# Optimization experiments

Hardware: AMD Instinct MI355X
Metric: run time of the kernel (lower is better)

The kernel has to match this reference:

```python
import jax, jax.numpy as jnp
import numpy as np

# ---- static configuration (mirrors scalar_python args) ----
N_SHOTS = 8
NZ = NX = 300
FD_PAD = 2                 # accuracy 4 -> fd_pad = accuracy // 2
NZP = NZ + 2 * FD_PAD      # 304
NXP = NX + 2 * FD_PAD      # 304
NT = 50
N_SRC = 1
N_REC = 300
DT = 0.001
DX = 4.0
INV_DX = 1.0 / DX
INV_DX2 = 1.0 / (DX * DX)
FLAT = NZP * NXP


def _shift(x, axis, s):
    """result[i] = x[i + s] along `axis`, zero-filled outside (matches padded-grid stencil)."""
    n = x.shape[axis]
    pad = [(0, 0)] * x.ndim
    if s > 0:
        xs = jax.lax.slice_in_dim(x, s, n, axis=axis)
        pad[axis] = (0, s)
    else:
        xs = jax.lax.slice_in_dim(x, 0, n + s, axis=axis)
        pad[axis] = (-s, 0)
    return jnp.pad(xs, pad)


def diff1(x, axis):
    """4th-order accurate central first derivative * (1/dx)."""
    return ((_shift(x, axis, 1) - _shift(x, axis, -1)) * (2.0 / 3.0)
            + (_shift(x, axis, -2) - _shift(x, axis, 2)) * (1.0 / 12.0)) * INV_DX


def diff2(x, axis):
    """4th-order accurate central second derivative * (1/dx^2)."""
    return ((-2.5) * x
            + (4.0 / 3.0) * (_shift(x, axis, 1) + _shift(x, axis, -1))
            - (1.0 / 12.0) * (_shift(x, axis, 2) + _shift(x, axis, -2))) * INV_DX2


def _forward_step(v2dt2, wfc, wfp, psi, zeta, a, b, dbdx):
    """One FDTD time step with PML (faithful to deepwave _forward_step, ndim=2)."""
    new_psi, new_zeta = [], []
    w_sum = jnp.zeros_like(wfc)
    for dim in range(2):          # dim 0 = z (axis 1), dim 1 = x (axis 2)
        axis = dim + 1
        dudx = diff1(wfc, axis)
        tmp = ((1.0 + b[dim]) * diff2(wfc, axis)
               + dbdx[dim] * dudx
               + diff1(a[dim] * psi[dim], axis))
        w_sum = w_sum + (1.0 + b[dim]) * tmp + a[dim] * zeta[dim]
        new_psi.append(b[dim] * dudx + a[dim] * psi[dim])
        new_zeta.append(b[dim] * tmp + a[dim] * zeta[dim])
    wfc_new = v2dt2 * w_sum + 2.0 * wfc - wfp
    return wfc_new, new_psi, new_zeta


def setup_inputs() -> dict:
    key = jax.random.key(0)
    ks = jax.random.split(key, 10)
    v = 1500.0 + 1000.0 * jax.random.uniform(ks[0], (NZP, NXP), jnp.float32)
    source_amplitudes = jax.random.normal(ks[1], (NT, N_SHOTS, N_SRC), jnp.float32)
    # PML profiles: (a, b, dbdx) per spatial dim, broadcastable 1D profiles.
    a_z = -0.1 * jax.random.uniform(ks[2], (NZP, 1), jnp.float32)
    b_z = 0.1 * jax.random.uniform(ks[3], (NZP, 1), jnp.float32)
    dbdx_z = 0.01 * jax.random.normal(ks[4], (NZP, 1), jnp.float32)
    a_x = -0.1 * jax.random.uniform(ks[5], (1, NXP), jnp.float32)
    b_x = 0.1 * jax.random.uniform(ks[6], (1, NXP), jnp.float32)
    dbdx_x = 0.01 * jax.random.normal(ks[7], (1, NXP), jnp.float32)
    sources_i = jax.random.randint(ks[8], (N_SHOTS, N_SRC), 0, FLAT, jnp.int32)
    receivers_i = jax.random.randint(ks[9], (N_SHOTS, N_REC), 0, FLAT, jnp.int32)
    return {"v": v, "source_amplitudes": source_amplitudes,
            "a_z": a_z, "b_z": b_z, "dbdx_z": dbdx_z,
            "a_x": a_x, "b_x": b_x, "dbdx_x": dbdx_x,
            "sources_i": sources_i, "receivers_i": receivers_i}


def reference(v, source_amplitudes, a_z, b_z, dbdx_z, a_x, b_x, dbdx_x,
              sources_i, receivers_i):
    v2dt2 = (v * v) * (DT * DT)                 # (NZP, NXP), broadcasts over shots
    a = (a_z, a_x)
    b = (b_z, b_x)
    dbdx = (dbdx_z, dbdx_x)
    shot_idx = jnp.arange(N_SHOTS)[:, None]
    zeros = jnp.zeros((N_SHOTS, NZP, NXP), v.dtype)

    def body(carry, amp_t):
        wfc, wfp, pz, px, zz, zx = carry
        # record receivers from the current wavefield (before the step)
        rec = jnp.take_along_axis(wfc.reshape(N_SHOTS, -1), receivers_i, axis=1)
        wfc_new, (pzn, pxn), (zzn, zxn) = _forward_step(
            v2dt2, wfc, wfp, (pz, px), (zz, zx), a, b, dbdx)
        # inject sources into the new wavefield (scatter-add of flat indices)
        flat = wfc_new.reshape(N_SHOTS, -1).at[shot_idx, sources_i].add(amp_t)
        wfc_new = flat.reshape(N_SHOTS, NZP, NXP)
        return (wfc_new, wfc, pzn, pxn, zzn, zxn), rec

    init = (zeros, zeros, zeros, zeros, zeros, zeros)
    _, receiver_amplitudes = jax.lax.scan(body, init, source_amplitudes)
    return receiver_amplitudes   # (NT, N_SHOTS, N_REC)
```

## Files before the change

### kernel.cpp

```cpp
#include <hip/hip_runtime.h>

#define N_SHOTS 8
#define NZP 304
#define NXP 304
#define NT 50
#define N_REC 300
#define FLAT (NZP * NXP)
#define DT 0.001f
#define INV_DX 0.25f
#define INV_DX2 0.0625f

#define C23 (2.0f / 3.0f)
#define C112 (1.0f / 12.0f)
#define C43 (4.0f / 3.0f)

#define NCH 361

union F4 { float4 v; float f[4]; };
__device__ __forceinline__ F4 ldf4(const float* p) {
    F4 r; r.v = *reinterpret_cast<const float4*>(p); return r;
}
__device__ __forceinline__ F4 zf4() {
    F4 r; r.v = make_float4(0.f, 0.f, 0.f, 0.f); return r;
}

__global__ __launch_bounds__(320) void fdtd_step4(
    const float* __restrict__ v,
    const float* __restrict__ amp,
    const float* __restrict__ az, const float* __restrict__ bz, const float* __restrict__ dbz,
    const float* __restrict__ ax, const float* __restrict__ bx, const float* __restrict__ dbx,
    const int* __restrict__ src_i,
    const int* __restrict__ rec_i,
    const float* __restrict__ wc,
    float* __restrict__ wp,
    const float* __restrict__ pzi, float* __restrict__ pzo,
    const float* __restrict__ pxi, float* __restrict__ pxo,
    float* __restrict__ zz, float* __restrict__ zx,
    float* __restrict__ rec_out,
    int t)
{
    const int bid = blockIdx.x;
    const int shot = bid & 7;
    const int j = bid >> 3;
    const int tid = threadIdx.x;
    const int sbase = shot * FLAT;

    if (tid >= NXP) {
        if (j < 19) {
            int ridx = j * 16 + (tid - NXP);
            if (ridx < N_REC) {
                rec_out[t * (N_SHOTS * N_REC) + shot * N_REC + ridx] =
                    wc[sbase + rec_i[shot * N_REC + ridx]];
            }
        }
        return;
    }

    const int srci = src_i[shot];
    const float amp_t = amp[t * N_SHOTS + shot];
    const int chbase = j * NCH;

    #pragma unroll
    for (int p = 0; p < 2; ++p) {
        const int chl = tid + 304 * p;
        if (p == 1 && tid >= NCH - 304) break;
        const int ch = chbase + chl;
        const int z = ch / 76;
        const int i = ch - z * 76;
        const int x0 = 4 * i;
        const int idx = sbase + 4 * ch;

        const bool lok = (i > 0), rok = (i < 75);
        F4 wCx = ldf4(wc + idx);
        F4 wLx = lok ? ldf4(wc + idx - 4) : zf4();
        F4 wRx = rok ? ldf4(wc + idx + 4) : zf4();
        F4 pCx = ldf4(pxi + idx);
        F4 pLx = lok ? ldf4(pxi + idx - 4) : zf4();
        F4 pRx = rok ? ldf4(pxi + idx + 4) : zf4();
        F4 aCx = ldf4(ax + x0);
        F4 aLx = lok ? ldf4(ax + x0 - 4) : zf4();
        F4 aRx = rok ? ldf4(ax + x0 + 4) : zf4();

        float wx[12], apx[12];
        #pragma unroll
        for (int k = 0; k < 4; ++k) {
            wx[k]     = wLx.f[k];  apx[k]     = aLx.f[k] * pLx.f[k];
            wx[4 + k] = wCx.f[k];  apx[4 + k] = aCx.f[k] * pCx.f[k];
            wx[8 + k] = wRx.f[k];  apx[8 + k] = aRx.f[k] * pRx.f[k];
        }

        const bool m1 = (z >= 1), m2 = (z >= 2), p1 = (z < NZP - 1), p2 = (z < NZP - 2);
        F4 wzm1 = m1 ? ldf4(wc + idx - NXP)     : zf4();
        F4 wzm2 = m2 ? ldf4(wc + idx - 2 * NXP) : zf4();
        F4 wzp1 = p1 ? ldf4(wc + idx + NXP)     : zf4();
        F4 wzp2 = p2 ? ldf4(wc + idx + 2 * NXP) : zf4();
        const float azm1 = m1 ? az[z - 1] : 0.f;
        const float azm2 = m2 ? az[z - 2] : 0.f;
        const float azp1 = p1 ? az[z + 1] : 0.f;
        const float azp2 = p2 ? az[z + 2] : 0.f;
        F4 qzm1 = m1 ? ldf4(pzi + idx - NXP)     : zf4();
        F4 qzm2 = m2 ? ldf4(pzi + idx - 2 * NXP) : zf4();
        F4 qzp1 = p1 ? ldf4(pzi + idx + NXP)     : zf4();
        F4 qzp2 = p2 ? ldf4(pzi + idx + 2 * NXP) : zf4();
        #pragma unroll
        for (int k = 0; k < 4; ++k) {
            qzm1.f[k] *= azm1; qzm2.f[k] *= azm2;
            qzp1.f[k] *= azp1; qzp2.f[k] *= azp2;
        }

        F4 pzC = ldf4(pzi + idx);
        F4 zzC = ldf4(zz + idx);
        F4 zxC = ldf4(zx + idx);
        F4 vC  = ldf4(v + 4 * ch);
        F4 wpC = ldf4(wp + idx);
        F4 bxC = ldf4(bx + x0);
        F4 dxC = ldf4(dbx + x0);
        const float azc = az[z], bzc = bz[z], dbzc = dbz[z];

        F4 o_w, o_pz, o_px, o_zz, o_zx;

        #pragma unroll
        for (int k = 0; k < 4; ++k) {
            const float c = wx[4 + k];
            const float d1x  = ((wx[5 + k] - wx[3 + k]) * C23 + (wx[2 + k] - wx[6 + k]) * C112) * INV_DX;
            const float d2x  = (-2.5f * c + C43 * (wx[5 + k] + wx[3 + k]) - C112 * (wx[6 + k] + wx[2 + k])) * INV_DX2;
            const float dapx = ((apx[5 + k] - apx[3 + k]) * C23 + (apx[2 + k] - apx[6 + k]) * C112) * INV_DX;
            const float d1z  = ((wzp1.f[k] - wzm1.f[k]) * C23 + (wzm2.f[k] - wzp2.f[k]) * C112) * INV_DX;
            const float d2z  = (-2.5f * c + C43 * (wzp1.f[k] + wzm1.f[k]) - C112 * (wzp2.f[k] + wzm2.f[k])) * INV_DX2;
            const float dapz = ((qzp1.f[k] - qzm1.f[k]) * C23 + (qzm2.f[k] - qzp2.f[k]) * C112) * INV_DX;

            const float tmpz = (1.f + bzc) * d2z + dbzc * d1z + dapz;
            float w_sum = (1.f + bzc) * tmpz + azc * zzC.f[k];

            const float bxk = bxC.f[k], axk = aCx.f[k];
            const float tmpx = (1.f + bxk) * d2x + dxC.f[k] * d1x + dapx;
            w_sum += (1.f + bxk) * tmpx + axk * zxC.f[k];

            const float vv = vC.f[k];
            float wn = (vv * vv) * (DT * DT) * w_sum + 2.f * c - wpC.f[k];
            if (4 * ch + k == srci) wn += amp_t;

            o_w.f[k]  = wn;
            o_pz.f[k] = bzc * d1z + azc * pzC.f[k];
            o_px.f[k] = bxk * d1x + apx[4 + k];
            o_zz.f[k] = bzc * tmpz + azc * zzC.f[k];
            o_zx.f[k] = bxk * tmpx + axk * zxC.f[k];
        }

        *reinterpret_cast<float4*>(wp + idx)  = o_w.v;
        *reinterpret_cast<float4*>(pzo + idx) = o_pz.v;
        *reinterpret_cast<float4*>(pxo + idx) = o_px.v;
        *reinterpret_cast<float4*>(zz + idx)  = o_zz.v;
        *reinterpret_cast<float4*>(zx + idx)  = o_zx.v;
    }
}

extern "C" void kernel_launch(void* const* d_in, const int* in_sizes, int n_in,
                              void* d_out, int out_size, void* d_ws, size_t ws_size,
                              hipStream_t stream) {
    const float* v     = (const float*)d_in[0];
    const float* amp   = (const float*)d_in[1];
    const float* az    = (const float*)d_in[2];
    const float* bz    = (const float*)d_in[3];
    const float* dbz   = (const float*)d_in[4];
    const float* ax    = (const float*)d_in[5];
    const float* bx    = (const float*)d_in[6];
    const float* dbx   = (const float*)d_in[7];
    const int* src_i   = (const int*)d_in[8];
    const int* rec_i   = (const int*)d_in[9];
    float* out = (float*)d_out;

    float* ws = (float*)d_ws;
    const size_t A = (size_t)N_SHOTS * FLAT;

    float* wf0 = ws + 0 * A; float* wf1 = ws + 1 * A;
    float* pz0 = ws + 2 * A; float* px0 = ws + 3 * A;
    float* zz  = ws + 4 * A; float* zx  = ws + 5 * A;
    float* pz1 = ws + 6 * A; float* px1 = ws + 7 * A;

    hipMemsetAsync(d_ws, 0, 6 * A * sizeof(float), stream);

    float* wf[2] = { wf0, wf1 };
    float* pz[2] = { pz0, pz1 };
    float* px[2] = { px0, px1 };

    int cur = 0;
    for (int t = 0; t < NT; ++t) {
        fdtd_step4<<<512, 320, 0, stream>>>(
            v, amp, az, bz, dbz, ax, bx, dbx, src_i, rec_i,
            wf[cur], wf[1 - cur],
            pz[cur], pz[1 - cur],
            px[cur], px[1 - cur],
            zz, zx, out, t);
        cur ^= 1;
    }
}
```

Before: 415.3 us.

## Store PML state pre-scaled by a, process two z-rows per thread, cache profiles in LDS

The kernel now keeps the auxiliary fields already multiplied by their PML coefficient a (q = a*psi, a*zeta), so stencil neighbours need no per-point a multiply and az/ax neighbour loads disappear. Each thread handles a 2-row by 4-column tile and reuses a 6-row z window of wavefield and qz loads across both rows, which cuts redundant global reads. The 1D PML profiles are staged in shared memory, and the block size drops to 192. The cost is a __syncthreads per block plus more registers per thread. Numerics shift slightly because the a scaling is folded into stored state.

```diff
diff --git a/kernel.cpp b/kernel.cpp
--- a/kernel.cpp
+++ b/kernel.cpp
@@ -14,7 +14,7 @@
 #define C112 (1.0f / 12.0f)
 #define C43 (4.0f / 3.0f)
 
-#define NCH 361
+#define TPS 11552
 
 union F4 { float4 v; float f[4]; };
 __device__ __forceinline__ F4 ldf4(const float* p) {
@@ -24,7 +24,7 @@
     F4 r; r.v = make_float4(0.f, 0.f, 0.f, 0.f); return r;
 }
 
-__global__ __launch_bounds__(320) void fdtd_step4(
+__global__ __launch_bounds__(192) void fdtd_stepq(
     const float* __restrict__ v,
     const float* __restrict__ amp,
     const float* __restrict__ az, const float* __restrict__ bz, const float* __restrict__ dbz,
@@ -33,125 +33,135 @@
     const int* __restrict__ rec_i,
     const float* __restrict__ wc,
     float* __restrict__ wp,
-    const float* __restrict__ pzi, float* __restrict__ pzo,
-    const float* __restrict__ pxi, float* __restrict__ pxo,
-    float* __restrict__ zz, float* __restrict__ zx,
+    const float* __restrict__ qzi, float* __restrict__ qzo,
+    const float* __restrict__ qxi, float* __restrict__ qxo,
+    float* __restrict__ azz, float* __restrict__ azx,
     float* __restrict__ rec_out,
     int t)
 {
+    __shared__ float laz[NZP], lbz[NZP], ldbz[NZP];
+    __shared__ float4 laxq[76], lbxq[76], ldbxq[76];
+
+    const int tid = threadIdx.x;
     const int bid = blockIdx.x;
     const int shot = bid & 7;
     const int j = bid >> 3;
-    const int tid = threadIdx.x;
     const int sbase = shot * FLAT;
 
-    if (tid >= NXP) {
-        if (j < 19) {
-            int ridx = j * 16 + (tid - NXP);
-            if (ridx < N_REC) {
-                rec_out[t * (N_SHOTS * N_REC) + shot * N_REC + ridx] =
-                    wc[sbase + rec_i[shot * N_REC + ridx]];
-            }
+    for (int p = tid; p < NZP; p += 192) {
+        laz[p] = az[p]; lbz[p] = bz[p]; ldbz[p] = dbz[p];
+    }
+    if (tid < 76) {
+        laxq[tid]  = *reinterpret_cast<const float4*>(ax + 4 * tid);
+        lbxq[tid]  = *reinterpret_cast<const float4*>(bx + 4 * tid);
+        ldbxq[tid] = *reinterpret_cast<const float4*>(dbx + 4 * tid);
+    }
+    __syncthreads();
+
+    if (tid >= 187) {
+        int ridx = j * 5 + (tid - 187);
+        if (ridx < N_REC) {
+            rec_out[t * (N_SHOTS * N_REC) + shot * N_REC + ridx] =
+                wc[sbase + rec_i[shot * N_REC + ridx]];
         }
         return;
     }
 
+    const int start = (j * TPS) >> 6;
+    const int count = (((j + 1) * TPS) >> 6) - start;
+    if (tid >= count) return;
+
+    const int c = start + tid;
+    const int m = c / 76;
+    const int i = c - m * 76;
+    const int z0 = 2 * m;
+    const int x0 = 4 * i;
+    const int idx0 = sbase + z0 * NXP + x0;
+
     const int srci = src_i[shot];
     const float amp_t = amp[t * N_SHOTS + shot];
-    const int chbase = j * NCH;
-
+
+    F4 wCw[6], qzw[6];
     #pragma unroll
-    for (int p = 0; p < 2; ++p) {
-        const int chl = tid + 304 * p;
-        if (p == 1 && tid >= NCH - 304) break;
-        const int ch = chbase + chl;
-        const int z = ch / 76;
-        const int i = ch - z * 76;
-        const int x0 = 4 * i;
-        const int idx = sbase + 4 * ch;
-
-        const bool lok = (i > 0), rok = (i < 75);
-        F4 wCx = ldf4(wc + idx);
-        F4 wLx = lok ? ldf4(wc + idx - 4) : zf4();
-        F4 wRx = rok ? ldf4(wc + idx + 4) : zf4();
-        F4 pCx = ldf4(pxi + idx);
-        F4 pLx = lok ? ldf4(pxi + idx - 4) : zf4();
-        F4 pRx = rok ? ldf4(pxi + idx + 4) : zf4();
-        F4 aCx = ldf4(ax + x0);
-        F4 aLx = lok ? ldf4(ax + x0 - 4) : zf4();
-        F4 aRx = rok ? ldf4(ax + x0 + 4) : zf4();
-
-        float wx[12], apx[12];
+    for (int r = 0; r < 6; ++r) {
+        const int zr = z0 - 2 + r;
+        const bool ok = (zr >= 0) && (zr < NZP);
+        const int a = sbase + zr * NXP + x0;
+        wCw[r] = ok ? ldf4(wc + a)  : zf4();
+        qzw[r] = ok ? ldf4(qzi + a) : zf4();
+    }
+
+    const bool lok = (i > 0), rok = (i < 75);
+    F4 wLr[2], wRr[2], qxL[2], qxC[2], qxR[2];
+    F4 vR[2], wpR[2], azzR[2], azxR[2];
+    #pragma unroll
+    for (int r = 0; r < 2; ++r) {
+        const int a = idx0 + r * NXP;
+        wLr[r] = lok ? ldf4(wc + a - 4)  : zf4();
+        wRr[r] = rok ? ldf4(wc + a + 4)  : zf4();
+        qxC[r] = ldf4(qxi + a);
+        qxL[r] = lok ? ldf4(qxi + a - 4) : zf4();
+        qxR[r] = rok ? ldf4(qxi + a + 4) : zf4();
+        vR[r]   = ldf4(v + (z0 + r) * NXP + x0);
+        wpR[r]  = ldf4(wp + a);
+        azzR[r] = ldf4(azz + a);
+        azxR[r] = ldf4(azx + a);
+    }
+
+    const F4 axv = *(F4*)&laxq[i];
+    const F4 bxv = *(F4*)&lbxq[i];
+    const F4 dxv = *(F4*)&ldbxq[i];
+
+    #pragma unroll
+    for (int r = 0; r < 2; ++r) {
+        const int z = z0 + r;
+        const int idx = idx0 + r * NXP;
+        const float azc = laz[z], bzc = lbz[z], dbzc = ldbz[z];
+        const float azbz = azc * bzc;
+
+        float wx[12], qxw[12];
         #pragma unroll
         for (int k = 0; k < 4; ++k) {
-            wx[k]     = wLx.f[k];  apx[k]     = aLx.f[k] * pLx.f[k];
-            wx[4 + k] = wCx.f[k];  apx[4 + k] = aCx.f[k] * pCx.f[k];
-            wx[8 + k] = wRx.f[k];  apx[8 + k] = aRx.f[k] * pRx.f[k];
+            wx[k]      = wLr[r].f[k];     qxw[k]     = qxL[r].f[k];
+            wx[4 + k]  = wCw[2 + r].f[k]; qxw[4 + k] = qxC[r].f[k];
+            wx[8 + k]  = wRr[r].f[k];     qxw[8 + k] = qxR[r].f[k];
         }
 
-        const bool m1 = (z >= 1), m2 = (z >= 2), p1 = (z < NZP - 1), p2 = (z < NZP - 2);
-        F4 wzm1 = m1 ? ldf4(wc + idx - NXP)     : zf4();
-        F4 wzm2 = m2 ? ldf4(wc + idx - 2 * NXP) : zf4();
-        F4 wzp1 = p1 ? ldf4(wc + idx + NXP)     : zf4();
-        F4 wzp2 = p2 ? ldf4(wc + idx + 2 * NXP) : zf4();
-        const float azm1 = m1 ? az[z - 1] : 0.f;
-        const float azm2 = m2 ? az[z - 2] : 0.f;
-        const float azp1 = p1 ? az[z + 1] : 0.f;
-        const float azp2 = p2 ? az[z + 2] : 0.f;
-        F4 qzm1 = m1 ? ldf4(pzi + idx - NXP)     : zf4();
-        F4 qzm2 = m2 ? ldf4(pzi + idx - 2 * NXP) : zf4();
-        F4 qzp1 = p1 ? ldf4(pzi + idx + NXP)     : zf4();
-        F4 qzp2 = p2 ? ldf4(pzi + idx + 2 * NXP) : zf4();
+        F4 o_w, o_qz, o_qx, o_zz, o_zx;
         #pragma unroll
         for (int k = 0; k < 4; ++k) {
-            qzm1.f[k] *= azm1; qzm2.f[k] *= azm2;
-            qzp1.f[k] *= azp1; qzp2.f[k] *= azp2;
+            const float cc = wx[4 + k];
+            const float d1x  = ((wx[5 + k] - wx[3 + k]) * C23 + (wx[2 + k] - wx[6 + k]) * C112) * INV_DX;
+            const float d2x  = (-2.5f * cc + C43 * (wx[5 + k] + wx[3 + k]) - C112 * (wx[6 + k] + wx[2 + k])) * INV_DX2;
+            const float dapx = ((qxw[5 + k] - qxw[3 + k]) * C23 + (qxw[2 + k] - qxw[6 + k]) * C112) * INV_DX;
+
+            const float d1z  = ((wCw[3 + r].f[k] - wCw[1 + r].f[k]) * C23 + (wCw[r].f[k] - wCw[4 + r].f[k]) * C112) * INV_DX;
+            const float d2z  = (-2.5f * cc + C43 * (wCw[3 + r].f[k] + wCw[1 + r].f[k]) - C112 * (wCw[4 + r].f[k] + wCw[r].f[k])) * INV_DX2;
+            const float dapz = ((qzw[3 + r].f[k] - qzw[1 + r].f[k]) * C23 + (qzw[r].f[k] - qzw[4 + r].f[k]) * C112) * INV_DX;
+
+            const float tmpz = (1.f + bzc) * d2z + dbzc * d1z + dapz;
+            float w_sum = (1.f + bzc) * tmpz + azzR[r].f[k];
+
+            const float bxk = bxv.f[k], axk = axv.f[k];
+            const float tmpx = (1.f + bxk) * d2x + dxv.f[k] * d1x + dapx;
+            w_sum += (1.f + bxk) * tmpx + azxR[r].f[k];
+
+            const float vv = vR[r].f[k];
+            float wn = (vv * vv) * (DT * DT) * w_sum + 2.f * cc - wpR[r].f[k];
+            if (z * NXP + x0 + k == srci) wn += amp_t;
+
+            o_w.f[k]  = wn;
+            o_qz.f[k] = azbz * d1z + azc * qzw[2 + r].f[k];
+            o_qx.f[k] = (axk * bxk) * d1x + axk * qxC[r].f[k];
+            o_zz.f[k] = azbz * tmpz + azc * azzR[r].f[k];
+            o_zx.f[k] = (axk * bxk) * tmpx + axk * azxR[r].f[k];
         }
 
-        F4 pzC = ldf4(pzi + idx);
-        F4 zzC = ldf4(zz + idx);
-        F4 zxC = ldf4(zx + idx);
-        F4 vC  = ldf4(v + 4 * ch);
-        F4 wpC = ldf4(wp + idx);
-        F4 bxC = ldf4(bx + x0);
-        F4 dxC = ldf4(dbx + x0);
-        const float azc = az[z], bzc = bz[z], dbzc = dbz[z];
-
-        F4 o_w, o_pz, o_px, o_zz, o_zx;
-
-        #pragma unroll
-        for (int k = 0; k < 4; ++k) {
-            const float c = wx[4 + k];
-            const float d1x  = ((wx[5 + k] - wx[3 + k]) * C23 + (wx[2 + k] - wx[6 + k]) * C112) * INV_DX;
-            const float d2x  = (-2.5f * c + C43 * (wx[5 + k] + wx[3 + k]) - C112 * (wx[6 + k] + wx[2 + k])) * INV_DX2;
-            const float dapx = ((apx[5 + k] - apx[3 + k]) * C23 + (apx[2 + k] - apx[6 + k]) * C112) * INV_DX;
-            const float d1z  = ((wzp1.f[k] - wzm1.f[k]) * C23 + (wzm2.f[k] - wzp2.f[k]) * C112) * INV_DX;
-            const float d2z  = (-2.5f * c + C43 * (wzp1.f[k] + wzm1.f[k]) - C112 * (wzp2.f[k] + wzm2.f[k])) * INV_DX2;
-            const float dapz = ((qzp1.f[k] - qzm1.f[k]) * C23 + (qzm2.f[k] - qzp2.f[k]) * C112) * INV_DX;
-
-            const float tmpz = (1.f + bzc) * d2z + dbzc * d1z + dapz;
-            float w_sum = (1.f + bzc) * tmpz + azc * zzC.f[k];
-
-            const float bxk = bxC.f[k], axk = aCx.f[k];
-            const float tmpx = (1.f + bxk) * d2x + dxC.f[k] * d1x + dapx;
-            w_sum += (1.f + bxk) * tmpx + axk * zxC.f[k];
-
-            const float vv = vC.f[k];
-            float wn = (vv * vv) * (DT * DT) * w_sum + 2.f * c - wpC.f[k];
-            if (4 * ch + k == srci) wn += amp_t;
-
-            o_w.f[k]  = wn;
-            o_pz.f[k] = bzc * d1z + azc * pzC.f[k];
-            o_px.f[k] = bxk * d1x + apx[4 + k];
-            o_zz.f[k] = bzc * tmpz + azc * zzC.f[k];
-            o_zx.f[k] = bxk * tmpx + axk * zxC.f[k];
-        }
-
         *reinterpret_cast<float4*>(wp + idx)  = o_w.v;
-        *reinterpret_cast<float4*>(pzo + idx) = o_pz.v;
-        *reinterpret_cast<float4*>(pxo + idx) = o_px.v;
-        *reinterpret_cast<float4*>(zz + idx)  = o_zz.v;
-        *reinterpret_cast<float4*>(zx + idx)  = o_zx.v;
+        *reinterpret_cast<float4*>(qzo + idx) = o_qz.v;
+        *reinterpret_cast<float4*>(qxo + idx) = o_qx.v;
+        *reinterpret_cast<float4*>(azz + idx) = o_zz.v;
+        *reinterpret_cast<float4*>(azx + idx) = o_zx.v;
     }
 }
 
@@ -174,24 +184,24 @@
     const size_t A = (size_t)N_SHOTS * FLAT;
 
     float* wf0 = ws + 0 * A; float* wf1 = ws + 1 * A;
-    float* pz0 = ws + 2 * A; float* px0 = ws + 3 * A;
-    float* zz  = ws + 4 * A; float* zx  = ws + 5 * A;
-    float* pz1 = ws + 6 * A; float* px1 = ws + 7 * A;
+    float* qz0 = ws + 2 * A; float* qx0 = ws + 3 * A;
+    float* azz = ws + 4 * A; float* azx = ws + 5 * A;
+    float* qz1 = ws + 6 * A; float* qx1 = ws + 7 * A;
 
     hipMemsetAsync(d_ws, 0, 6 * A * sizeof(float), stream);
 
     float* wf[2] = { wf0, wf1 };
-    float* pz[2] = { pz0, pz1 };
-    float* px[2] = { px0, px1 };
+    float* qz[2] = { qz0, qz1 };
+    float* qx[2] = { qx0, qx1 };
 
     int cur = 0;
     for (int t = 0; t < NT; ++t) {
-        fdtd_step4<<<512, 320, 0, stream>>>(
+        fdtd_stepq<<<512, 192, 0, stream>>>(
             v, amp, az, bz, dbz, ax, bx, dbx, src_i, rec_i,
             wf[cur], wf[1 - cur],
-            pz[cur], pz[1 - cur],
-            px[cur], px[1 - cur],
-            zz, zx, out, t);
+            qz[cur], qz[1 - cur],
+            qx[cur], qx[1 - cur],
+            azz, azx, out, t);
         cur ^= 1;
     }
 }
```

Result: slower. 479.1 us (+15.4%).
